# Kernel optimization log

Measured on AMD Instinct MI355X. Metric: run time of the kernel, lower is better.

## Reference

```python
import jax, jax.numpy as jnp
import numpy as np

B, C, H, W = 8, 64, 256, 256
N_HEADS = 4
MODES_X, MODES_Y = 32, 32 // 2 + 1  # rfft half-spectrum along last dim
O_PER_HEAD = C // N_HEADS


def setup_inputs() -> dict:
    key = jax.random.key(0)
    k1, k2, k3 = jax.random.split(key, 3)
    x = jax.random.normal(k1, (B, C, H, W), dtype=jnp.float32)
    weights_real = jax.random.normal(k2, (N_HEADS, C, O_PER_HEAD, MODES_X, MODES_Y), dtype=jnp.float32) * 0.01
    weights_imag = jax.random.normal(k3, (N_HEADS, C, O_PER_HEAD, MODES_X, MODES_Y), dtype=jnp.float32) * 0.01
    bias = jnp.zeros((C, 1, 1), dtype=jnp.float32)
    return {"x": x, "weights_real": weights_real, "weights_imag": weights_imag, "bias": bias}


def reference(x, weights_real, weights_imag, bias):
    b, c, h, w = x.shape
    nh, _, o, mxw, myw = weights_real.shape
    # rfft2 with ortho norm, matching torch.fft.rfft2(..., norm='ortho')
    xf = jnp.fft.rfft2(x, norm="ortho")  # [B, C, H, W//2+1] complex64
    fH, fW = xf.shape[-2], xf.shape[-1]
    mx = min(mxw, fH)
    my = min(myw, fW)
    wgt = weights_real[..., :mx, :my] + 1j * weights_imag[..., :mx, :my]  # [nh, C, o, mx, my]
    # all heads at once: torch loop 'biXY,ioXY->boXY' per head == 'bixy,hioxy->bhoxy'
    prod = jnp.einsum("bixy,hioxy->bhoxy", xf[:, :, :mx, :my], wgt)  # [B, nh, o, mx, my]
    out_f = jnp.zeros((b, nh, o, fH, fW), dtype=prod.dtype).at[..., :mx, :my].set(prod)
    out = jnp.fft.irfft2(out_f, s=(h, w), norm="ortho")  # [B, nh, o, H, W] real
    # torch.cat over heads along channel dim == head-major reshape
    out = out.reshape(b, nh * o, h, w)
    return out + bias  # bias [C,1,1] broadcasts
```

## Files before the change

kernel.cpp:

```cpp
#include <hip/hip_runtime.h>
#include <hip/hip_bf16.h>

#define NROWS 131072
#define MY 17
#define MX 32


#define K1_ROWS 30
#define NCHUNK 9

__global__ __launch_bounds__(256) void f1_fw(const float* __restrict__ x,
                                             float2* __restrict__ X2) {
    __shared__ __align__(16) float s_lds[4][K1_ROWS][68];
    __shared__ float2 xs[4352];
    int t = threadIdx.x;
    int bc = blockIdx.x;
    const float* xp = x + (long)bc * 65536;

    int j = t % 17;
    int g = t / 17;
    int r0 = g * 2;
    int odd = j & 1;
    float ca = odd ? 0.f : ((j & 2) ? -1.f : 1.f);
    float cb = odd ? (((j & 3) == 1) ? -1.f : 1.f) : 0.f;
    float cj, sj;
    sincospif((float)j * (1.0f / 128.0f), &sj, &cj);
    sj = -sj;
    float swv, cwv;
    sincospif((float)j * 0.25f, &swv, &cwv);
    swv = -swv;
    float k1c = cwv * ca - swv * cb;
    float k2c = swv * ca + cwv * cb;
    const float4* A4 = (const float4*)&s_lds[odd ? 1 : 0][0][0] + r0 * 17;
    const float4* B4 = (const float4*)&s_lds[odd ? 3 : 2][0][0] + r0 * 17;

    float4 q0[2], q1[2], q2[2], q3[2];

#define F1_REGLOAD(cc)                                                         \
    {                                                                          \
        int nr_ = ((cc) < 8) ? K1_ROWS : 16;                                   \
        int items_ = nr_ * 16;                                                 \
        _Pragma("unroll")                                                      \
        for (int i = 0; i < 2; ++i) {                                          \
            int item = i * 256 + t;                                            \
            int it = item < items_ ? item : items_ - 1;                        \
            int r = it >> 4, cq = it & 15;                                     \
            const float4* xr =                                                 \
                (const float4*)(xp + ((cc) * K1_ROWS + r) * 256) + cq;         \
            q0[i] = xr[0];                                                     \
            q1[i] = xr[16];                                                    \
            q2[i] = xr[32];                                                    \
            q3[i] = xr[48];                                                    \
        }                                                                      \
    }

    F1_REGLOAD(0)

    for (int c = 0; c < NCHUNK; ++c) {
        int nr = (c < 8) ? K1_ROWS : 16;
        int items = nr * 16;

#pragma unroll
        for (int i = 0; i < 2; ++i) {
            int item = i * 256 + t;
            if (item < items) {
                int r = item >> 4, cq = item & 15;
                float4 s02p, s02m, s13p, s13m;
                s02p.x = q0[i].x + q2[i].x; s02p.y = q0[i].y + q2[i].y;
                s02p.z = q0[i].z + q2[i].z; s02p.w = q0[i].w + q2[i].w;
                s02m.x = q0[i].x - q2[i].x; s02m.y = q0[i].y - q2[i].y;
                s02m.z = q0[i].z - q2[i].z; s02m.w = q0[i].w - q2[i].w;
                s13p.x = q1[i].x + q3[i].x; s13p.y = q1[i].y + q3[i].y;
                s13p.z = q1[i].z + q3[i].z; s13p.w = q1[i].w + q3[i].w;
                s13m.x = q1[i].x - q3[i].x; s13m.y = q1[i].y - q3[i].y;
                s13m.z = q1[i].z - q3[i].z; s13m.w = q1[i].w - q3[i].w;
                *(float4*)&s_lds[0][r][cq * 4] = s02p;
                *(float4*)&s_lds[1][r][cq * 4] = s02m;
                *(float4*)&s_lds[2][r][cq * 4] = s13p;
                *(float4*)&s_lds[3][r][cq * 4] = s13m;
            }
        }
        __syncthreads();

        if (c + 1 < NCHUNK) F1_REGLOAD(c + 1)

        if (t < 255 && r0 + 2 <= nr) {
            float pc = 1.f, ps = 0.f;
            float ar0 = 0, ai0 = 0, ar1 = 0, ai1 = 0;

#define K1_STEP(a0e, b0e, a0f, b0f, a1e, b1e, a1f, b1f)               \
  { float t0re = fmaf(k1c, (b0f), fmaf(cwv, (a0f), fmaf(ca, (b0e), (a0e)))); \
    float t0im = fmaf(k2c, (b0f), fmaf(swv, (a0f), cb * (b0e)));      \
    float t1re = fmaf(k1c, (b1f), fmaf(cwv, (a1f), fmaf(ca, (b1e), (a1e)))); \
    float t1im = fmaf(k2c, (b1f), fmaf(swv, (a1f), cb * (b1e)));      \
    ar0 = fmaf(t0re, pc, ar0); ar0 = fmaf(-t0im, ps, ar0);            \
    ai0 = fmaf(t0re, ps, ai0); ai0 = fmaf(t0im, pc, ai0);             \
    ar1 = fmaf(t1re, pc, ar1); ar1 = fmaf(-t1im, ps, ar1);            \
    ai1 = fmaf(t1re, ps, ai1); ai1 = fmaf(t1im, pc, ai1);             \
    float nps = fmaf(pc, sj, ps * cj);                                \
    pc = fmaf(pc, cj, -(ps * sj)); ps = nps; }

#pragma unroll 2
            for (int l4 = 0; l4 < 8; ++l4) {
                float4 va0 = A4[l4], vb0 = B4[l4];
                float4 vA0 = A4[8 + l4], vB0 = B4[8 + l4];
                float4 va1 = A4[17 + l4], vb1 = B4[17 + l4];
                float4 vA1 = A4[25 + l4], vB1 = B4[25 + l4];
                K1_STEP(va0.x, vb0.x, vA0.x, vB0.x, va1.x, vb1.x, vA1.x, vB1.x)
                K1_STEP(va0.y, vb0.y, vA0.y, vB0.y, va1.y, vb1.y, vA1.y, vB1.y)
                K1_STEP(va0.z, vb0.z, vA0.z, vB0.z, va1.z, vb1.z, vA1.z, vB1.z)
                K1_STEP(va0.w, vb0.w, vA0.w, vB0.w, va1.w, vb1.w, vA1.w, vB1.w)
            }
#undef K1_STEP

            int h = c * K1_ROWS + r0;
            xs[h * 17 + j] = make_float2(ar0, ai0);
            xs[(h + 1) * 17 + j] = make_float2(ar1, ai1);
        }
        __syncthreads();
    }

    for (int q = t; q < 2176; q += 256) {
        float2 a = xs[q], b = xs[q + 2176];
        xs[q] = make_float2(a.x + b.x, a.y + b.y);
        xs[q + 2176] = make_float2(a.x - b.x, a.y - b.y);
    }
    __syncthreads();

    for (int q = t; q < 544; q += 256) {
        int kx = q / 17, ky = q % 17;
        int kodd = kx & 1;
        float cA = kodd ? 0.f : ((kx & 2) ? -1.f : 1.f);
        float cB = kodd ? (((kx & 3) == 1) ? -1.f : 1.f) : 0.f;
        float cBn = -cB;
        const float2* Aq = xs + (kodd ? 2176 : 0) + ky;
        float cs, ss;
        sincospif((float)kx * (1.0f / 128.0f), &ss, &cs);
        ss = -ss;
        float pc = 1.f, psn = 0.f;
        float ar = 0.f, ai = 0.f;
#pragma unroll 4
        for (int m = 0; m < 64; ++m) {
            float2 a = Aq[m * 17];
            float2 b = Aq[1088 + m * 17];
            float yre = fmaf(cBn, b.y, fmaf(cA, b.x, a.x));
            float yim = fmaf(cB, b.x, fmaf(cA, b.y, a.y));
            ar = fmaf(yre, pc, ar); ar = fmaf(-yim, psn, ar);
            ai = fmaf(yre, psn, ai); ai = fmaf(yim, pc, ai);
            float npc = pc * cs - psn * ss;
            psn = pc * ss + psn * cs;
            pc = npc;
        }
        X2[(long)bc * 544 + q] = make_float2(ar, ai);
    }
#undef F1_REGLOAD
}

__global__ __launch_bounds__(256) void k3_mix(const float2* __restrict__ X2,
                                              const float* __restrict__ wr_g,
                                              const float* __restrict__ wi_g,
                                              float2* __restrict__ P) {
    __shared__ float2 xsh[544];
    __shared__ float2 wsh[4352];
    int t = threadIdx.x;
    int bi = blockIdx.x;
    int kx = bi & 31;
    int bh = (bi >> 5) & 3;
    int n = bi >> 7;

    float accr0 = 0, acci0 = 0, accr1 = 0, acci1 = 0, accr2 = 0, acci2 = 0;

    for (int ic = 0; ic < 4; ++ic) {
        __syncthreads();
        for (int q = t; q < 544; q += 256) {
            int ii = q / 34;
            int rem = q % 34;
            int b = rem / 17;
            int ky = rem % 17;
            int i = ic * 16 + ii;
            xsh[q] = X2[((long)((bh * 2 + b) * 64 + i) * 32 + kx) * 17 + ky];
        }
        for (int q = t; q < 4352; q += 256) {
            int ii = q / 272;
            int rem = q % 272;
            int o = rem / 17;
            int ky = rem % 17;
            int i = ic * 16 + ii;
            long widx = ((long)((n * 64 + i) * 16 + o)) * 544 + kx * 17 + ky;
            wsh[q] = make_float2(wr_g[widx], wi_g[widx]);
        }
        __syncthreads();

#pragma unroll 3
        for (int rep = 0; rep < 3; ++rep) {
            int q = t + rep * 256;
            if (q < 544) {
                int ky = q % 17;
                int o = (q / 17) & 15;
                int b = q / 272;
                float ar = 0.f, ai = 0.f;
#pragma unroll
                for (int ii = 0; ii < 16; ++ii) {
                    float2 xv = xsh[ii * 34 + b * 17 + ky];
                    float2 wv = wsh[ii * 272 + o * 17 + ky];
                    ar += xv.x * wv.x - xv.y * wv.y;
                    ai += xv.x * wv.y + xv.y * wv.x;
                }
                if (rep == 0) { accr0 += ar; acci0 += ai; }
                else if (rep == 1) { accr1 += ar; acci1 += ai; }
                else { accr2 += ar; acci2 += ai; }
            }
        }
    }

    {
        int q = t;
        int ky = q % 17, o = (q / 17) & 15, b = q / 272;
        int ch = (bh * 2 + b) * 64 + n * 16 + o;
        P[((long)ch * 32 + kx) * 17 + ky] = make_float2(accr0, acci0);
    }
    {
        int q = t + 256;
        int ky = q % 17, o = (q / 17) & 15, b = q / 272;
        int ch = (bh * 2 + b) * 64 + n * 16 + o;
        P[((long)ch * 32 + kx) * 17 + ky] = make_float2(accr1, acci1);
    }
    if (t < 32) {
        int q = t + 512;
        int ky = q % 17, o = (q / 17) & 15, b = q / 272;
        int ch = (bh * 2 + b) * 64 + n * 16 + o;
        P[((long)ch * 32 + kx) * 17 + ky] = make_float2(accr2, acci2);
    }
}

__global__ __launch_bounds__(256) void f2_inv(const float2* __restrict__ P,
                                              const float* __restrict__ bias,
                                              float* __restrict__ out) {
    __shared__ float2 psh[544];
    __shared__ float2 zsh[4352];
    int t = threadIdx.x;
    int plane = blockIdx.x;
    long base = (long)plane * 544;
    psh[t] = P[base + t];
    psh[t + 256] = P[base + t + 256];
    if (t < 32) psh[t + 512] = P[base + t + 512];
    __syncthreads();

    {
        float chh, shh;
        sincospif((float)t * (1.0f / 128.0f), &shh, &chh);
        float pc = 1.f, psn = 0.f;
        float ar[17], ai[17];
#pragma unroll
        for (int ky = 0; ky < 17; ++ky) { ar[ky] = 0.f; ai[ky] = 0.f; }

        for (int kx = 0; kx < 32; ++kx) {
#pragma unroll
            for (int ky = 0; ky < 17; ++ky) {
                float2 v = psh[kx * 17 + ky];
                ar[ky] += v.x * pc - v.y * psn;
                ai[ky] += v.x * psn + v.y * pc;
            }
            float npc = pc * chh - psn * shh;
            psn = pc * shh + psn * chh;
            pc = npc;
        }
#pragma unroll
        for (int ky = 0; ky < 17; ++ky) zsh[t * 17 + ky] = make_float2(ar[ky], ai[ky]);
    }
    __syncthreads();

    int wv = t >> 6;
    int lane = t & 63;
    float bv = bias[plane & 63];
    float c0, s0;
    sincospif((float)lane * (1.0f / 128.0f), &s0, &c0);
    const float inv = 1.0f / 65536.0f;
    const float inv2 = 2.0f / 65536.0f;
    long ob_plane = (long)plane * 65536;

    for (int it8 = 0; it8 < 32; ++it8) {
        int r0 = it8 * 8 + wv * 2;
        float pc = c0, psn = s0;
        float a00 = 0, a01 = 0, a02 = 0, a03 = 0;
        float a10 = 0, a11 = 0, a12 = 0, a13 = 0;

#pragma unroll
        for (int ky = 1; ky <= 16; ++ky) {
            float2 z0 = zsh[r0 * 17 + ky];
            float2 z1 = zsh[(r0 + 1) * 17 + ky];
            float A0 = z0.x * pc - z0.y * psn;
            float B0 = z0.x * psn + z0.y * pc;
            float A1 = z1.x * pc - z1.y * psn;
            float B1 = z1.x * psn + z1.y * pc;
            a00 += A0; a10 += A1;
            a01 += ((ky & 3) == 0) ? A0 : ((ky & 3) == 1) ? -B0 : ((ky & 3) == 2) ? -A0 : B0;
            a11 += ((ky & 3) == 0) ? A1 : ((ky & 3) == 1) ? -B1 : ((ky & 3) == 2) ? -A1 : B1;
            a02 += (ky & 1) ? -A0 : A0;
            a12 += (ky & 1) ? -A1 : A1;
            a03 += ((ky & 3) == 0) ? A0 : ((ky & 3) == 1) ? B0 : ((ky & 3) == 2) ? -A0 : -B0;
            a13 += ((ky & 3) == 0) ? A1 : ((ky & 3) == 1) ? B1 : ((ky & 3) == 2) ? -A1 : -B1;
            float npc = pc * c0 - psn * s0;
            psn = pc * s0 + psn * c0;
            pc = npc;
        }
        float base0 = zsh[r0 * 17].x * inv + bv;
        float base1 = zsh[(r0 + 1) * 17].x * inv + bv;
        long ob0 = ob_plane + (long)r0 * 256;
        long ob1 = ob0 + 256;
        out[ob0 + lane]       = fmaf(a00, inv2, base0);
        out[ob0 + 64 + lane]  = fmaf(a01, inv2, base0);
        out[ob0 + 128 + lane] = fmaf(a02, inv2, base0);
        out[ob0 + 192 + lane] = fmaf(a03, inv2, base0);
        out[ob1 + lane]       = fmaf(a10, inv2, base1);
        out[ob1 + 64 + lane]  = fmaf(a11, inv2, base1);
        out[ob1 + 128 + lane] = fmaf(a12, inv2, base1);
        out[ob1 + 192 + lane] = fmaf(a13, inv2, base1);
    }
}

extern "C" void kernel_launch(void* const* d_in, const int* in_sizes, int n_in,
                              void* d_out, int out_size, void* d_ws, size_t ws_size,
                              hipStream_t stream) {
    const float* x = (const float*)d_in[0];
    const float* wr = (const float*)d_in[1];
    const float* wi = (const float*)d_in[2];
    const float* bias = (const float*)d_in[3];
    float* out = (float*)d_out;
    float* ws = (float*)d_ws;

    float2* X2 = (float2*)(ws + 4456960);
    float2* P  = (float2*)(ws + 5014016);

    hipLaunchKernelGGL(f1_fw, dim3(512), dim3(256), 0, stream, x, X2);
    hipLaunchKernelGGL(k3_mix, dim3(512), dim3(256), 0, stream, X2, wr, wi, P);
    hipLaunchKernelGGL(f2_inv, dim3(512), dim3(256), 0, stream, P, bias, out);
}
```

Measured before the change: 121.1 us.

## Double thread count in forward and inverse FFT kernels to raise parallelism

Both f1_fw and f2_inv now launch 512 threads per block instead of 256. The forward kernel gives each thread one row instead of two, and the inverse kernel splits the 17 ky columns across two thread halves and handles 16 rows per iteration. With only 512 blocks on a large GPU, this aims to put more waves in flight and hide latency. In exchange, per-thread ILP drops and the maximum register budget per thread shrinks, which could cause spilling.

```diff
diff --git a/kernel.cpp b/kernel.cpp
--- a/kernel.cpp
+++ b/kernel.cpp
@@ -9,7 +9,7 @@
 #define K1_ROWS 30
 #define NCHUNK 9
 
-__global__ __launch_bounds__(256) void f1_fw(const float* __restrict__ x,
+__global__ __launch_bounds__(512) void f1_fw(const float* __restrict__ x,
                                              float2* __restrict__ X2) {
     __shared__ __align__(16) float s_lds[4][K1_ROWS][68];
     __shared__ float2 xs[4352];
@@ -18,8 +18,8 @@
     const float* xp = x + (long)bc * 65536;
 
     int j = t % 17;
-    int g = t / 17;
-    int r0 = g * 2;
+    int r = t / 17;
+    int rc = r < K1_ROWS ? r : 0;
     int odd = j & 1;
     float ca = odd ? 0.f : ((j & 2) ? -1.f : 1.f);
     float cb = odd ? (((j & 3) == 1) ? -1.f : 1.f) : 0.f;
@@ -31,27 +31,23 @@
     swv = -swv;
     float k1c = cwv * ca - swv * cb;
     float k2c = swv * ca + cwv * cb;
-    const float4* A4 = (const float4*)&s_lds[odd ? 1 : 0][0][0] + r0 * 17;
-    const float4* B4 = (const float4*)&s_lds[odd ? 3 : 2][0][0] + r0 * 17;
-
-    float4 q0[2], q1[2], q2[2], q3[2];
+    const float4* A4 = (const float4*)&s_lds[odd ? 1 : 0][rc][0];
+    const float4* B4 = (const float4*)&s_lds[odd ? 3 : 2][rc][0];
+
+    float4 q0, q1, q2, q3;
 
 #define F1_REGLOAD(cc)                                                         \
     {                                                                          \
         int nr_ = ((cc) < 8) ? K1_ROWS : 16;                                   \
         int items_ = nr_ * 16;                                                 \
-        _Pragma("unroll")                                                      \
-        for (int i = 0; i < 2; ++i) {                                          \
-            int item = i * 256 + t;                                            \
-            int it = item < items_ ? item : items_ - 1;                        \
-            int r = it >> 4, cq = it & 15;                                     \
-            const float4* xr =                                                 \
-                (const float4*)(xp + ((cc) * K1_ROWS + r) * 256) + cq;         \
-            q0[i] = xr[0];                                                     \
-            q1[i] = xr[16];                                                    \
-            q2[i] = xr[32];                                                    \
-            q3[i] = xr[48];                                                    \
-        }                                                                      \
+        int it = t < items_ ? t : items_ - 1;                                  \
+        int rr = it >> 4, cq = it & 15;                                        \
+        const float4* xr =                                                     \
+            (const float4*)(xp + ((cc) * K1_ROWS + rr) * 256) + cq;            \
+        q0 = xr[0];                                                            \
+        q1 = xr[16];                                                           \
+        q2 = xr[32];                                                           \
+        q3 = xr[48];                                                           \
     }
 
     F1_REGLOAD(0)
@@ -60,43 +56,35 @@
         int nr = (c < 8) ? K1_ROWS : 16;
         int items = nr * 16;
 
-#pragma unroll
-        for (int i = 0; i < 2; ++i) {
-            int item = i * 256 + t;
-            if (item < items) {
-                int r = item >> 4, cq = item & 15;
-                float4 s02p, s02m, s13p, s13m;
-                s02p.x = q0[i].x + q2[i].x; s02p.y = q0[i].y + q2[i].y;
-                s02p.z = q0[i].z + q2[i].z; s02p.w = q0[i].w + q2[i].w;
-                s02m.x = q0[i].x - q2[i].x; s02m.y = q0[i].y - q2[i].y;
-                s02m.z = q0[i].z - q2[i].z; s02m.w = q0[i].w - q2[i].w;
-                s13p.x = q1[i].x + q3[i].x; s13p.y = q1[i].y + q3[i].y;
-                s13p.z = q1[i].z + q3[i].z; s13p.w = q1[i].w + q3[i].w;
-                s13m.x = q1[i].x - q3[i].x; s13m.y = q1[i].y - q3[i].y;
-                s13m.z = q1[i].z - q3[i].z; s13m.w = q1[i].w - q3[i].w;
-                *(float4*)&s_lds[0][r][cq * 4] = s02p;
-                *(float4*)&s_lds[1][r][cq * 4] = s02m;
-                *(float4*)&s_lds[2][r][cq * 4] = s13p;
-                *(float4*)&s_lds[3][r][cq * 4] = s13m;
-            }
+        if (t < items) {
+            int rr = t >> 4, cq = t & 15;
+            float4 s02p, s02m, s13p, s13m;
+            s02p.x = q0.x + q2.x; s02p.y = q0.y + q2.y;
+            s02p.z = q0.z + q2.z; s02p.w = q0.w + q2.w;
+            s02m.x = q0.x - q2.x; s02m.y = q0.y - q2.y;
+            s02m.z = q0.z - q2.z; s02m.w = q0.w - q2.w;
+            s13p.x = q1.x + q3.x; s13p.y = q1.y + q3.y;
+            s13p.z = q1.z + q3.z; s13p.w = q1.w + q3.w;
+            s13m.x = q1.x - q3.x; s13m.y = q1.y - q3.y;
+            s13m.z = q1.z - q3.z; s13m.w = q1.w - q3.w;
+            *(float4*)&s_lds[0][rr][cq * 4] = s02p;
+            *(float4*)&s_lds[1][rr][cq * 4] = s02m;
+            *(float4*)&s_lds[2][rr][cq * 4] = s13p;
+            *(float4*)&s_lds[3][rr][cq * 4] = s13m;
         }
         __syncthreads();
 
         if (c + 1 < NCHUNK) F1_REGLOAD(c + 1)
 
-        if (t < 255 && r0 + 2 <= nr) {
+        if (t < 510 && r < nr) {
             float pc = 1.f, ps = 0.f;
-            float ar0 = 0, ai0 = 0, ar1 = 0, ai1 = 0;
-
-#define K1_STEP(a0e, b0e, a0f, b0f, a1e, b1e, a1f, b1f)               \
+            float ar0 = 0, ai0 = 0;
+
+#define K1_STEP(a0e, b0e, a0f, b0f)                                   \
   { float t0re = fmaf(k1c, (b0f), fmaf(cwv, (a0f), fmaf(ca, (b0e), (a0e)))); \
     float t0im = fmaf(k2c, (b0f), fmaf(swv, (a0f), cb * (b0e)));      \
-    float t1re = fmaf(k1c, (b1f), fmaf(cwv, (a1f), fmaf(ca, (b1e), (a1e)))); \
-    float t1im = fmaf(k2c, (b1f), fmaf(swv, (a1f), cb * (b1e)));      \
     ar0 = fmaf(t0re, pc, ar0); ar0 = fmaf(-t0im, ps, ar0);            \
     ai0 = fmaf(t0re, ps, ai0); ai0 = fmaf(t0im, pc, ai0);             \
-    ar1 = fmaf(t1re, pc, ar1); ar1 = fmaf(-t1im, ps, ar1);            \
-    ai1 = fmaf(t1re, ps, ai1); ai1 = fmaf(t1im, pc, ai1);             \
     float nps = fmaf(pc, sj, ps * cj);                                \
     pc = fmaf(pc, cj, -(ps * sj)); ps = nps; }
 
@@ -104,30 +92,27 @@
             for (int l4 = 0; l4 < 8; ++l4) {
                 float4 va0 = A4[l4], vb0 = B4[l4];
                 float4 vA0 = A4[8 + l4], vB0 = B4[8 + l4];
-                float4 va1 = A4[17 + l4], vb1 = B4[17 + l4];
-                float4 vA1 = A4[25 + l4], vB1 = B4[25 + l4];
-                K1_STEP(va0.x, vb0.x, vA0.x, vB0.x, va1.x, vb1.x, vA1.x, vB1.x)
-                K1_STEP(va0.y, vb0.y, vA0.y, vB0.y, va1.y, vb1.y, vA1.y, vB1.y)
-                K1_STEP(va0.z, vb0.z, vA0.z, vB0.z, va1.z, vb1.z, vA1.z, vB1.z)
-                K1_STEP(va0.w, vb0.w, vA0.w, vB0.w, va1.w, vb1.w, vA1.w, vB1.w)
+                K1_STEP(va0.x, vb0.x, vA0.x, vB0.x)
+                K1_STEP(va0.y, vb0.y, vA0.y, vB0.y)
+                K1_STEP(va0.z, vb0.z, vA0.z, vB0.z)
+                K1_STEP(va0.w, vb0.w, vA0.w, vB0.w)
             }
 #undef K1_STEP
 
-            int h = c * K1_ROWS + r0;
+            int h = c * K1_ROWS + r;
             xs[h * 17 + j] = make_float2(ar0, ai0);
-            xs[(h + 1) * 17 + j] = make_float2(ar1, ai1);
         }
         __syncthreads();
     }
 
-    for (int q = t; q < 2176; q += 256) {
+    for (int q = t; q < 2176; q += 512) {
         float2 a = xs[q], b = xs[q + 2176];
         xs[q] = make_float2(a.x + b.x, a.y + b.y);
         xs[q + 2176] = make_float2(a.x - b.x, a.y - b.y);
     }
     __syncthreads();
 
-    for (int q = t; q < 544; q += 256) {
+    for (int q = t; q < 544; q += 512) {
         int kx = q / 17, ky = q % 17;
         int kodd = kx & 1;
         float cA = kodd ? 0.f : ((kx & 2) ? -1.f : 1.f);
@@ -233,7 +218,7 @@
     }
 }
 
-__global__ __launch_bounds__(256) void f2_inv(const float2* __restrict__ P,
+__global__ __launch_bounds__(512) void f2_inv(const float2* __restrict__ P,
                                               const float* __restrict__ bias,
                                               float* __restrict__ out) {
     __shared__ float2 psh[544];
@@ -241,32 +226,38 @@
     int t = threadIdx.x;
     int plane = blockIdx.x;
     long base = (long)plane * 544;
-    psh[t] = P[base + t];
-    psh[t + 256] = P[base + t + 256];
-    if (t < 32) psh[t + 512] = P[base + t + 512];
+    for (int q = t; q < 544; q += 512) psh[q] = P[base + q];
     __syncthreads();
 
     {
+        int h = t & 255;
+        int half = t >> 8;
+        int kyb = half ? 9 : 0;
+        int cnt = half ? 8 : 9;
         float chh, shh;
-        sincospif((float)t * (1.0f / 128.0f), &shh, &chh);
+        sincospif((float)h * (1.0f / 128.0f), &shh, &chh);
         float pc = 1.f, psn = 0.f;
-        float ar[17], ai[17];
-#pragma unroll
-        for (int ky = 0; ky < 17; ++ky) { ar[ky] = 0.f; ai[ky] = 0.f; }
-
+        float ar[9], ai[9];
+#pragma unroll
+        for (int u = 0; u < 9; ++u) { ar[u] = 0.f; ai[u] = 0.f; }
+
+        const float2* pq = psh + kyb;
         for (int kx = 0; kx < 32; ++kx) {
 #pragma unroll
-            for (int ky = 0; ky < 17; ++ky) {
-                float2 v = psh[kx * 17 + ky];
-                ar[ky] += v.x * pc - v.y * psn;
-                ai[ky] += v.x * psn + v.y * pc;
+            for (int u = 0; u < 9; ++u) {
+                if (u < cnt) {
+                    float2 v = pq[kx * 17 + u];
+                    ar[u] += v.x * pc - v.y * psn;
+                    ai[u] += v.x * psn + v.y * pc;
+                }
             }
             float npc = pc * chh - psn * shh;
             psn = pc * shh + psn * chh;
             pc = npc;
         }
 #pragma unroll
-        for (int ky = 0; ky < 17; ++ky) zsh[t * 17 + ky] = make_float2(ar[ky], ai[ky]);
+        for (int u = 0; u < 9; ++u)
+            if (u < cnt) zsh[h * 17 + kyb + u] = make_float2(ar[u], ai[u]);
     }
     __syncthreads();
 
@@ -279,8 +270,8 @@
     const float inv2 = 2.0f / 65536.0f;
     long ob_plane = (long)plane * 65536;
 
-    for (int it8 = 0; it8 < 32; ++it8) {
-        int r0 = it8 * 8 + wv * 2;
+    for (int it16 = 0; it16 < 16; ++it16) {
+        int r0 = it16 * 16 + wv * 2;
         float pc = c0, psn = s0;
         float a00 = 0, a01 = 0, a02 = 0, a03 = 0;
         float a10 = 0, a11 = 0, a12 = 0, a13 = 0;
@@ -332,7 +323,7 @@
     float2* X2 = (float2*)(ws + 4456960);
     float2* P  = (float2*)(ws + 5014016);
 
-    hipLaunchKernelGGL(f1_fw, dim3(512), dim3(256), 0, stream, x, X2);
+    hipLaunchKernelGGL(f1_fw, dim3(512), dim3(512), 0, stream, x, X2);
     hipLaunchKernelGGL(k3_mix, dim3(512), dim3(256), 0, stream, X2, wr, wi, P);
-    hipLaunchKernelGGL(f2_inv, dim3(512), dim3(256), 0, stream, P, bias, out);
+    hipLaunchKernelGGL(f2_inv, dim3(512), dim3(512), 0, stream, P, bias, out);
 }
```

After: 120.6 us. About the same (-0.4%).
